# Kernel optimization log

Measured on AMD Instinct MI355X. Metric: run time of the kernel, lower is better.

The kernel has to match this reference:

```python
import jax, jax.numpy as jnp
import numpy as np

B, T, C_IN, H, W = 128, 12, 10, 25, 25
HID = 64
DN = ('NCHW', 'OIHW', 'NCHW')


def setup_inputs() -> dict:
    key = jax.random.key(0)
    ks = jax.random.split(key, 8)
    x = jax.random.normal(ks[0], (B, T, C_IN, H, W), dtype=jnp.float32)
    # ConvLSTM cell: conv over concat([x, h]) -> 4*HID gate channels, 3x3 kernel
    conv_w = jax.random.normal(ks[1], (4 * HID, C_IN + HID, 3, 3), dtype=jnp.float32) * 0.05
    conv_b = jnp.zeros((4 * HID,), dtype=jnp.float32)
    # MLP head: hidden*25*25 -> 16 -> 8 -> 2
    w1 = jax.random.normal(ks[2], (HID * H * W, 16), dtype=jnp.float32) * 0.01
    b1 = jnp.zeros((16,), dtype=jnp.float32)
    w2 = jax.random.normal(ks[3], (16, 8), dtype=jnp.float32) * 0.1
    b2 = jnp.zeros((8,), dtype=jnp.float32)
    w3 = jax.random.normal(ks[4], (8, 2), dtype=jnp.float32) * 0.1
    b3 = jnp.zeros((2,), dtype=jnp.float32)
    return {"x": x, "conv_w": conv_w, "conv_b": conv_b,
            "w1": w1, "b1": b1, "w2": w2, "b2": b2, "w3": w3, "b3": b3}


def _convlstm_last_h(x, conv_w, conv_b):
    # x: (B,T,C,H,W); returns last hidden state h_T: (B,HID,H,W)
    h0 = jnp.zeros((x.shape[0], HID, H, W), dtype=x.dtype)
    c0 = jnp.zeros_like(h0)

    def step(carry, xt):
        h, c = carry
        inp = jnp.concatenate([xt, h], axis=1)              # (B, C+HID, H, W)
        gates = jax.lax.conv_general_dilated(
            inp, conv_w, window_strides=(1, 1), padding='SAME',
            dimension_numbers=DN) + conv_b[None, :, None, None]  # (B,4*HID,H,W)
        i, f, o, g = jnp.split(gates, 4, axis=1)
        i, f, o = jax.nn.sigmoid(i), jax.nn.sigmoid(f), jax.nn.sigmoid(o)
        g = jnp.tanh(g)
        c_new = f * c + i * g
        h_new = o * jnp.tanh(c_new)
        return (h_new, c_new), None

    (h_last, _), _ = jax.lax.scan(step, (h0, c0), jnp.swapaxes(x, 0, 1))
    return h_last


def reference(x, conv_w, conv_b, w1, b1, w2, b2, w3, b3):
    h = _convlstm_last_h(x, conv_w, conv_b)          # (B,HID,25,25)
    h = jax.nn.relu(h).reshape(h.shape[0], -1)       # flatten
    # dropout is identity in eval mode
    h = jax.nn.relu(h @ w1 + b1)
    h = jax.nn.relu(h @ w2 + b2)
    logits = h @ w3 + b3                             # (B,2)
    return jax.nn.log_softmax(logits, axis=1)
```

## Files before the change

kernel.cpp:

```cpp
#include <hip/hip_runtime.h>
#include <hip/hip_bf16.h>
#include <math.h>

#define BATCH 128
#define TT    12
#define CIN   10
#define HID   64
#define PLANE 625
#define NU    10
#define IPB   50000
#define NKB   45
#define CSZ   (BATCH*PLANE*HID)
#define KSPLIT 10

typedef __attribute__((ext_vector_type(8)))  short bf16x8;
typedef __attribute__((ext_vector_type(16))) float f32x16;

__device__ __forceinline__ float fsigm(float v){ return 1.f/(1.f+__expf(-v)); }
__device__ __forceinline__ float ftanh(float v){ return 1.f - 2.f/(__expf(2.f*v)+1.f); }
__device__ __forceinline__ unsigned short f2bf(float v){
    __hip_bfloat16 b = __float2bfloat16(v);
    return *reinterpret_cast<unsigned short*>(&b);
}

__global__ void k_wprep(const float* __restrict__ w, unsigned short* __restrict__ wpk){
    int tid = blockIdx.x*256 + threadIdx.x;
    if (tid >= NKB*8*64) return;
    int lane = tid & 63;
    int nt   = (tid >> 6) & 7;
    int kb   = tid >> 9;
    int tap = kb/5, ci = kb - tap*5;
    int ky = tap/3, kx = tap - ky*3;
    int g = lane & 3, jlo = (lane & 31) >> 2, kh = lane >> 5;
    int o = g*64 + nt*8 + jlo;
    union { unsigned short u[8]; float4 f; } pk;
    #pragma unroll
    for (int e = 0; e < 8; ++e){
        int ch = ci*16 + kh*8 + e;
        float v = (ch < 74) ? w[((o*74 + ch)*3 + ky)*3 + kx] : 0.f;
        pk.u[e] = f2bf(v);
    }
    *reinterpret_cast<float4*>(wpk + (size_t)tid*8) = pk.f;
}

__global__ void k_xcopy(const float* __restrict__ x, unsigned short* __restrict__ inp, int t){
    int idx = blockIdx.x*256 + threadIdx.x;
    if (idx >= BATCH*CIN*PLANE) return;
    int m  = idx % PLANE;
    int r  = idx / PLANE;
    int ch = r % CIN;
    int b  = r / CIN;
    float v = x[((size_t)(b*TT + t)*CIN + ch)*PLANE + m];
    inp[(size_t)b*IPB + ((((ch>>3)*PLANE) + m)<<3) + (ch&7)] = f2bf(v);
}

__global__ __launch_bounds__(512) void k_gemm(
    const float* __restrict__ x,
    const unsigned short* __restrict__ inp,
    unsigned short* __restrict__ inpn,
    const unsigned short* __restrict__ wpk,
    const float* __restrict__ bias,
    float* __restrict__ cbuf,
    float* __restrict__ hbuf,
    int t)
{
    __shared__ __align__(16) unsigned short at2[2160*8];

    const int tid  = threadIdx.x;
    const int mg   = blockIdx.x;
    const int b    = blockIdx.y;
    const int lane = tid & 63;
    const int nt   = tid >> 6;
    const int r0row = (mg*128)/25;

    const unsigned short* ib = inp + (size_t)b*IPB;
    for (int idx = tid; idx < 2160; idx += 512){
        int q   = idx/216, pix = idx - q*216;
        int rr  = pix/27,  cc  = pix - rr*27;
        int gr  = r0row - 1 + rr, gc = cc - 1;
        float4 v = {0.f,0.f,0.f,0.f};
        if ((unsigned)gr < 25u && (unsigned)gc < 25u)
            v = *reinterpret_cast<const float4*>(ib + (((size_t)q*PLANE + gr*25 + gc)<<3));
        *reinterpret_cast<float4*>(at2 + ((size_t)idx<<3)) = v;
    }

    const int kh = lane >> 5;
    const unsigned short* ap[4];
    #pragma unroll
    for (int mt = 0; mt < 4; ++mt){
        int m = mg*128 + mt*32 + (lane & 31);
        int row = m/25, col = m - row*25;
        int pm = (row - r0row + 1)*27 + col;
        ap[mt] = at2 + ((kh*216 + pm - 27) << 3);
    }

    f32x16 acc[4];
    #pragma unroll
    for (int mt = 0; mt < 4; ++mt)
        #pragma unroll
        for (int e = 0; e < 16; ++e) acc[mt][e] = 0.f;

    __syncthreads();

    const bf16x8* wptr = reinterpret_cast<const bf16x8*>(wpk) + nt*64 + lane;
    bf16x8 bcur = *wptr;
    const unsigned short *a0 = ap[0], *a1 = ap[1], *a2 = ap[2], *a3 = ap[3];
    #pragma unroll 1
    for (int tap = 0; tap < 9; ++tap){
        #pragma unroll
        for (int ci = 0; ci < 5; ++ci){
            bf16x8 bnxt = wptr[512];
            wptr += 512;
            bf16x8 f0 = *reinterpret_cast<const bf16x8*>(a0 + ci*3456);
            bf16x8 f1 = *reinterpret_cast<const bf16x8*>(a1 + ci*3456);
            bf16x8 f2 = *reinterpret_cast<const bf16x8*>(a2 + ci*3456);
            bf16x8 f3 = *reinterpret_cast<const bf16x8*>(a3 + ci*3456);
            acc[0] = __builtin_amdgcn_mfma_f32_32x32x16_bf16(f0, bcur, acc[0], 0,0,0);
            acc[1] = __builtin_amdgcn_mfma_f32_32x32x16_bf16(f1, bcur, acc[1], 0,0,0);
            acc[2] = __builtin_amdgcn_mfma_f32_32x32x16_bf16(f2, bcur, acc[2], 0,0,0);
            acc[3] = __builtin_amdgcn_mfma_f32_32x32x16_bf16(f3, bcur, acc[3], 0,0,0);
            bcur = bnxt;
        }
        const int d = (tap == 2 || tap == 5) ? 25*8 : 8;
        a0 += d; a1 += d; a2 += d; a3 += d;
    }

    const int g   = lane & 3;
    const int jlo = (lane & 31) >> 2;
    const int j   = nt*8 + jlo;
    const float bown = bias[g*64 + j];
    const float sA = (g == 3) ? 2.f : 1.f;
    const float sB = (g == 3) ? -1.f : 0.f;
    const int  mbase = mg*128 + 4*kh;
    const bool gb0 = (g & 1), gb1 = (g & 2);
    float* cb = cbuf + (size_t)b*PLANE*HID;
    float* hb = hbuf + (size_t)b*PLANE*HID;
    unsigned short* hn = inpn + (size_t)b*IPB;
    const int chh = CIN + j, uh = chh >> 3, sh = chh & 7;

    #pragma unroll
    for (int mt = 0; mt < 4; ++mt){
        #pragma unroll
        for (int rq = 0; rq < 4; ++rq){
            float v0 = fmaf(sA, fsigm(sA*(acc[mt][rq*4+0] + bown)), sB);
            float v1 = fmaf(sA, fsigm(sA*(acc[mt][rq*4+1] + bown)), sB);
            float v2 = fmaf(sA, fsigm(sA*(acc[mt][rq*4+2] + bown)), sB);
            float v3 = fmaf(sA, fsigm(sA*(acc[mt][rq*4+3] + bown)), sB);
            float s;
            s = __shfl_xor(gb0 ? v0 : v1, 1); if (gb0) v0 = s; else v1 = s;
            s = __shfl_xor(gb0 ? v2 : v3, 1); if (gb0) v2 = s; else v3 = s;
            s = __shfl_xor(gb1 ? v0 : v2, 2); if (gb1) v0 = s; else v2 = s;
            s = __shfl_xor(gb1 ? v1 : v3, 2); if (gb1) v1 = s; else v3 = s;
            const int m = mbase + mt*32 + g + 8*rq;
            if (m < PLANE){
                float co = cb[m*HID + j];
                float cn = fmaf(v1, co, v0*v3);
                float h  = v2 * ftanh(cn);
                cb[m*HID + j] = cn;
                hn[((uh*PLANE + m) << 3) + sh] = f2bf(h);
                if (t == TT-1) hb[m*HID + j] = h;
            }
        }
    }

    if (t < TT-1){
        const float* xn = x + (size_t)(b*TT + t + 1)*CIN*PLANE;
        for (int idx = tid; idx < 1280; idx += 512){
            int ch = idx >> 7, mi = idx & 127;
            int m = mg*128 + mi;
            if (m < PLANE)
                inpn[(size_t)b*IPB + ((((ch>>3)*PLANE) + m)<<3) + (ch&7)] =
                    f2bf(xn[ch*PLANE + m]);
        }
    }
}

__global__ __launch_bounds__(256) void k_mlp1(
    const float* __restrict__ hfin, const float* __restrict__ w1,
    float* __restrict__ part)
{
    __shared__ float xw[4][16];
    const int ks = blockIdx.x, b = blockIdx.y, tid = threadIdx.x;
    const float* hbb = hfin + (size_t)b * (HID * PLANE);

    float acc[16];
    #pragma unroll
    for (int i = 0; i < 16; ++i) acc[i] = 0.f;

    const int kw0 = ks * 4000, kw1 = kw0 + 4000;
    for (int kw = kw0 + tid; kw < kw1; kw += 256){
        int j = kw / 625, m = kw - j * 625;
        float hv = hbb[m * 64 + j];
        hv = hv > 0.f ? hv : 0.f;
        const float4* wf = (const float4*)(w1 + (size_t)kw * 16);
        float4 wa = wf[0], wb = wf[1], wc = wf[2], wd = wf[3];
        acc[ 0] = fmaf(hv, wa.x, acc[ 0]); acc[ 1] = fmaf(hv, wa.y, acc[ 1]);
        acc[ 2] = fmaf(hv, wa.z, acc[ 2]); acc[ 3] = fmaf(hv, wa.w, acc[ 3]);
        acc[ 4] = fmaf(hv, wb.x, acc[ 4]); acc[ 5] = fmaf(hv, wb.y, acc[ 5]);
        acc[ 6] = fmaf(hv, wb.z, acc[ 6]); acc[ 7] = fmaf(hv, wb.w, acc[ 7]);
        acc[ 8] = fmaf(hv, wc.x, acc[ 8]); acc[ 9] = fmaf(hv, wc.y, acc[ 9]);
        acc[10] = fmaf(hv, wc.z, acc[10]); acc[11] = fmaf(hv, wc.w, acc[11]);
        acc[12] = fmaf(hv, wd.x, acc[12]); acc[13] = fmaf(hv, wd.y, acc[13]);
        acc[14] = fmaf(hv, wd.z, acc[14]); acc[15] = fmaf(hv, wd.w, acc[15]);
    }
    #pragma unroll
    for (int d = 1; d < 64; d <<= 1)
        #pragma unroll
        for (int i = 0; i < 16; ++i) acc[i] += __shfl_xor(acc[i], d);
    if ((tid & 63) == 0)
        #pragma unroll
        for (int i = 0; i < 16; ++i) xw[tid >> 6][i] = acc[i];
    __syncthreads();
    if (tid < 16)
        part[((size_t)b * KSPLIT + ks) * 16 + tid] =
            xw[0][tid] + xw[1][tid] + xw[2][tid] + xw[3][tid];
}

__global__ __launch_bounds__(128) void k_mlp2(
    const float* __restrict__ part,
    const float* __restrict__ b1,
    const float* __restrict__ w2, const float* __restrict__ b2,
    const float* __restrict__ w3, const float* __restrict__ b3,
    float* __restrict__ out)
{
    const int b = threadIdx.x;
    float h1[16];
    #pragma unroll
    for (int i = 0; i < 16; ++i) h1[i] = b1[i];
    for (int s = 0; s < KSPLIT; ++s)
        #pragma unroll
        for (int i = 0; i < 16; ++i) h1[i] += part[((size_t)b * KSPLIT + s) * 16 + i];
    #pragma unroll
    for (int i = 0; i < 16; ++i) h1[i] = h1[i] > 0.f ? h1[i] : 0.f;

    float h2[8];
    #pragma unroll
    for (int i = 0; i < 8; ++i){
        float s2 = b2[i];
        #pragma unroll
        for (int k2 = 0; k2 < 16; ++k2) s2 += h1[k2] * w2[k2*8 + i];
        h2[i] = s2 > 0.f ? s2 : 0.f;
    }
    float l0 = b3[0], l1 = b3[1];
    #pragma unroll
    for (int k3 = 0; k3 < 8; ++k3){ l0 += h2[k3]*w3[k3*2]; l1 += h2[k3]*w3[k3*2+1]; }
    float m   = fmaxf(l0, l1);
    float lse = m + logf(__expf(l0 - m) + __expf(l1 - m));
    out[b*2 + 0] = l0 - lse;
    out[b*2 + 1] = l1 - lse;
}

extern "C" void kernel_launch(void* const* d_in, const int* in_sizes, int n_in,
                              void* d_out, int out_size, void* d_ws, size_t ws_size,
                              hipStream_t stream) {
    const float* x      = (const float*)d_in[0];
    const float* conv_w = (const float*)d_in[1];
    const float* conv_b = (const float*)d_in[2];
    const float* w1     = (const float*)d_in[3];
    const float* b1     = (const float*)d_in[4];
    const float* w2     = (const float*)d_in[5];
    const float* b2     = (const float*)d_in[6];
    const float* w3     = (const float*)d_in[7];
    const float* b3     = (const float*)d_in[8];
    float* out = (float*)d_out;

    unsigned short* inp0 = (unsigned short*)d_ws;
    unsigned short* inp1 = inp0 + (size_t)BATCH*IPB;
    float* c   = (float*)(inp1 + (size_t)BATCH*IPB);
    float* hb  = c + CSZ;
    unsigned short* wpk = (unsigned short*)(hb + CSZ);
    float* part = (float*)(wpk + (size_t)(NKB+1)*8*64*8);

    hipMemsetAsync(inp0, 0, (size_t)BATCH*IPB*2, stream);
    hipMemsetAsync(inp1, 0, (size_t)BATCH*IPB*2, stream);
    hipMemsetAsync(c,    0, (size_t)CSZ*4,       stream);

    k_wprep<<<dim3(90),   dim3(256), 0, stream>>>(conv_w, wpk);
    k_xcopy<<<dim3(3125), dim3(256), 0, stream>>>(x, inp0, 0);

    for (int t = 0; t < TT; ++t){
        unsigned short* ic  = (t & 1) ? inp1 : inp0;
        unsigned short* in_ = (t & 1) ? inp0 : inp1;
        k_gemm<<<dim3(5, BATCH), dim3(512), 0, stream>>>(x, ic, in_, wpk, conv_b, c, hb, t);
    }
    k_mlp1<<<dim3(KSPLIT, BATCH), dim3(256), 0, stream>>>(hb, w1, part);
    k_mlp2<<<dim3(1), dim3(128), 0, stream>>>(part, b1, w2, b2, w3, b3, out);
}
```

Before: 732.9 us.

## Halve gemm pixel tile, store bf16 relu'd final h, batch MLP1 over four samples

The ConvLSTM gemm now covers 64 pixels per block instead of 128, doubling the grid to 10x128 blocks and shrinking the LDS tile. This raises occupancy and parallelism for the recurrent step. The last timestep writes only a bf16, ReLU-applied hidden state in pixel-major order and skips the useless c/h updates. w1 is pre-permuted to match that layout, so k_mlp1 reads it contiguously and reuses each weight load across four batch samples. The costs are more halo reloads per block and an extra prep kernel, plus bf16 rounding of the MLP input.

```diff
diff --git a/kernel.cpp b/kernel.cpp
--- a/kernel.cpp
+++ b/kernel.cpp
@@ -43,6 +43,15 @@
     *reinterpret_cast<float4*>(wpk + (size_t)tid*8) = pk.f;
 }
 
+__global__ void k_w1prep(const float* __restrict__ w1, float* __restrict__ w1t){
+    int tid = blockIdx.x*256 + threadIdx.x;
+    if (tid >= 40000*4) return;
+    int rowp = tid >> 2, f4 = tid & 3;
+    int m = rowp >> 6, j = rowp & 63;
+    const float4* src = (const float4*)(w1 + (size_t)(j*625 + m)*16);
+    ((float4*)(w1t + (size_t)rowp*16))[f4] = src[f4];
+}
+
 __global__ void k_xcopy(const float* __restrict__ x, unsigned short* __restrict__ inp, int t){
     int idx = blockIdx.x*256 + threadIdx.x;
     if (idx >= BATCH*CIN*PLANE) return;
@@ -61,23 +70,23 @@
     const unsigned short* __restrict__ wpk,
     const float* __restrict__ bias,
     float* __restrict__ cbuf,
-    float* __restrict__ hbuf,
+    unsigned short* __restrict__ hbf,
     int t)
 {
-    __shared__ __align__(16) unsigned short at2[2160*8];
+    __shared__ __align__(16) unsigned short at2[1620*8];
 
     const int tid  = threadIdx.x;
     const int mg   = blockIdx.x;
     const int b    = blockIdx.y;
     const int lane = tid & 63;
     const int nt   = tid >> 6;
-    const int r0row = (mg*128)/25;
+    const int rlo  = (mg*64)/25;
 
     const unsigned short* ib = inp + (size_t)b*IPB;
-    for (int idx = tid; idx < 2160; idx += 512){
-        int q   = idx/216, pix = idx - q*216;
+    for (int idx = tid; idx < 1620; idx += 512){
+        int q   = idx/162, pix = idx - q*162;
         int rr  = pix/27,  cc  = pix - rr*27;
-        int gr  = r0row - 1 + rr, gc = cc - 1;
+        int gr  = rlo - 1 + rr, gc = cc - 1;
         float4 v = {0.f,0.f,0.f,0.f};
         if ((unsigned)gr < 25u && (unsigned)gc < 25u)
             v = *reinterpret_cast<const float4*>(ib + (((size_t)q*PLANE + gr*25 + gc)<<3));
@@ -85,18 +94,18 @@
     }
 
     const int kh = lane >> 5;
-    const unsigned short* ap[4];
-    #pragma unroll
-    for (int mt = 0; mt < 4; ++mt){
-        int m = mg*128 + mt*32 + (lane & 31);
+    const unsigned short* ap[2];
+    #pragma unroll
+    for (int mt = 0; mt < 2; ++mt){
+        int m = mg*64 + mt*32 + (lane & 31);
         int row = m/25, col = m - row*25;
-        int pm = (row - r0row + 1)*27 + col;
-        ap[mt] = at2 + ((kh*216 + pm - 27) << 3);
-    }
-
-    f32x16 acc[4];
-    #pragma unroll
-    for (int mt = 0; mt < 4; ++mt)
+        int pm = (row - rlo + 1)*27 + col;
+        ap[mt] = at2 + kh*1296 + ((pm - 27) << 3);
+    }
+
+    f32x16 acc[2];
+    #pragma unroll
+    for (int mt = 0; mt < 2; ++mt)
         #pragma unroll
         for (int e = 0; e < 16; ++e) acc[mt][e] = 0.f;
 
@@ -104,25 +113,21 @@
 
     const bf16x8* wptr = reinterpret_cast<const bf16x8*>(wpk) + nt*64 + lane;
     bf16x8 bcur = *wptr;
-    const unsigned short *a0 = ap[0], *a1 = ap[1], *a2 = ap[2], *a3 = ap[3];
+    const unsigned short *a0 = ap[0], *a1 = ap[1];
     #pragma unroll 1
     for (int tap = 0; tap < 9; ++tap){
         #pragma unroll
         for (int ci = 0; ci < 5; ++ci){
             bf16x8 bnxt = wptr[512];
             wptr += 512;
-            bf16x8 f0 = *reinterpret_cast<const bf16x8*>(a0 + ci*3456);
-            bf16x8 f1 = *reinterpret_cast<const bf16x8*>(a1 + ci*3456);
-            bf16x8 f2 = *reinterpret_cast<const bf16x8*>(a2 + ci*3456);
-            bf16x8 f3 = *reinterpret_cast<const bf16x8*>(a3 + ci*3456);
+            bf16x8 f0 = *reinterpret_cast<const bf16x8*>(a0 + ci*2592);
+            bf16x8 f1 = *reinterpret_cast<const bf16x8*>(a1 + ci*2592);
             acc[0] = __builtin_amdgcn_mfma_f32_32x32x16_bf16(f0, bcur, acc[0], 0,0,0);
             acc[1] = __builtin_amdgcn_mfma_f32_32x32x16_bf16(f1, bcur, acc[1], 0,0,0);
-            acc[2] = __builtin_amdgcn_mfma_f32_32x32x16_bf16(f2, bcur, acc[2], 0,0,0);
-            acc[3] = __builtin_amdgcn_mfma_f32_32x32x16_bf16(f3, bcur, acc[3], 0,0,0);
             bcur = bnxt;
         }
         const int d = (tap == 2 || tap == 5) ? 25*8 : 8;
-        a0 += d; a1 += d; a2 += d; a3 += d;
+        a0 += d; a1 += d;
     }
 
     const int g   = lane & 3;
@@ -131,15 +136,15 @@
     const float bown = bias[g*64 + j];
     const float sA = (g == 3) ? 2.f : 1.f;
     const float sB = (g == 3) ? -1.f : 0.f;
-    const int  mbase = mg*128 + 4*kh;
+    const int  mbase = mg*64 + 4*kh;
     const bool gb0 = (g & 1), gb1 = (g & 2);
     float* cb = cbuf + (size_t)b*PLANE*HID;
-    float* hb = hbuf + (size_t)b*PLANE*HID;
-    unsigned short* hn = inpn + (size_t)b*IPB;
+    unsigned short* hn  = inpn + (size_t)b*IPB;
+    unsigned short* hfb = hbf  + (size_t)b*40000;
     const int chh = CIN + j, uh = chh >> 3, sh = chh & 7;
 
     #pragma unroll
-    for (int mt = 0; mt < 4; ++mt){
+    for (int mt = 0; mt < 2; ++mt){
         #pragma unroll
         for (int rq = 0; rq < 4; ++rq){
             float v0 = fmaf(sA, fsigm(sA*(acc[mt][rq*4+0] + bown)), sB);
@@ -156,18 +161,21 @@
                 float co = cb[m*HID + j];
                 float cn = fmaf(v1, co, v0*v3);
                 float h  = v2 * ftanh(cn);
-                cb[m*HID + j] = cn;
-                hn[((uh*PLANE + m) << 3) + sh] = f2bf(h);
-                if (t == TT-1) hb[m*HID + j] = h;
+                if (t < TT-1){
+                    cb[m*HID + j] = cn;
+                    hn[((uh*PLANE + m) << 3) + sh] = f2bf(h);
+                } else {
+                    hfb[m*64 + j] = f2bf(h > 0.f ? h : 0.f);
+                }
             }
         }
     }
 
     if (t < TT-1){
         const float* xn = x + (size_t)(b*TT + t + 1)*CIN*PLANE;
-        for (int idx = tid; idx < 1280; idx += 512){
-            int ch = idx >> 7, mi = idx & 127;
-            int m = mg*128 + mi;
+        for (int idx = tid; idx < 640; idx += 512){
+            int ch = idx >> 6, mi = idx & 63;
+            int m = mg*64 + mi;
             if (m < PLANE)
                 inpn[(size_t)b*IPB + ((((ch>>3)*PLANE) + m)<<3) + (ch&7)] =
                     f2bf(xn[ch*PLANE + m]);
@@ -176,44 +184,73 @@
 }
 
 __global__ __launch_bounds__(256) void k_mlp1(
-    const float* __restrict__ hfin, const float* __restrict__ w1,
+    const unsigned short* __restrict__ hbf, const float* __restrict__ w1t,
     float* __restrict__ part)
 {
-    __shared__ float xw[4][16];
-    const int ks = blockIdx.x, b = blockIdx.y, tid = threadIdx.x;
-    const float* hbb = hfin + (size_t)b * (HID * PLANE);
-
-    float acc[16];
-    #pragma unroll
-    for (int i = 0; i < 16; ++i) acc[i] = 0.f;
-
-    const int kw0 = ks * 4000, kw1 = kw0 + 4000;
-    for (int kw = kw0 + tid; kw < kw1; kw += 256){
-        int j = kw / 625, m = kw - j * 625;
-        float hv = hbb[m * 64 + j];
-        hv = hv > 0.f ? hv : 0.f;
-        const float4* wf = (const float4*)(w1 + (size_t)kw * 16);
-        float4 wa = wf[0], wb = wf[1], wc = wf[2], wd = wf[3];
-        acc[ 0] = fmaf(hv, wa.x, acc[ 0]); acc[ 1] = fmaf(hv, wa.y, acc[ 1]);
-        acc[ 2] = fmaf(hv, wa.z, acc[ 2]); acc[ 3] = fmaf(hv, wa.w, acc[ 3]);
-        acc[ 4] = fmaf(hv, wb.x, acc[ 4]); acc[ 5] = fmaf(hv, wb.y, acc[ 5]);
-        acc[ 6] = fmaf(hv, wb.z, acc[ 6]); acc[ 7] = fmaf(hv, wb.w, acc[ 7]);
-        acc[ 8] = fmaf(hv, wc.x, acc[ 8]); acc[ 9] = fmaf(hv, wc.y, acc[ 9]);
-        acc[10] = fmaf(hv, wc.z, acc[10]); acc[11] = fmaf(hv, wc.w, acc[11]);
-        acc[12] = fmaf(hv, wd.x, acc[12]); acc[13] = fmaf(hv, wd.y, acc[13]);
-        acc[14] = fmaf(hv, wd.z, acc[14]); acc[15] = fmaf(hv, wd.w, acc[15]);
-    }
+    __shared__ float xw[4][4][16];
+    const int ks = blockIdx.x, bg = blockIdx.y, tid = threadIdx.x;
+    const int kw0 = ks*4000, kw1 = kw0 + 4000;
+    const unsigned short* h0 = hbf + (size_t)(bg*4+0)*40000;
+    const unsigned short* h1 = hbf + (size_t)(bg*4+1)*40000;
+    const unsigned short* h2 = hbf + (size_t)(bg*4+2)*40000;
+    const unsigned short* h3 = hbf + (size_t)(bg*4+3)*40000;
+
+    float acc[4][16];
+    #pragma unroll
+    for (int bi = 0; bi < 4; ++bi)
+        #pragma unroll
+        for (int n = 0; n < 16; ++n) acc[bi][n] = 0.f;
+
+    for (int kw = kw0 + tid*2; kw < kw1; kw += 512){
+        const float4* wp = (const float4*)(w1t + (size_t)kw*16);
+        float4 q0 = wp[0], q1 = wp[1], q2 = wp[2], q3 = wp[3];
+        float4 r0 = wp[4], r1 = wp[5], r2 = wp[6], r3 = wp[7];
+        unsigned int u0 = *(const unsigned int*)(h0 + kw);
+        unsigned int u1 = *(const unsigned int*)(h1 + kw);
+        unsigned int u2 = *(const unsigned int*)(h2 + kw);
+        unsigned int u3 = *(const unsigned int*)(h3 + kw);
+        #define ACC1(bi, u) { \
+            float fl = __uint_as_float((u) << 16); \
+            float fh = __uint_as_float((u) & 0xffff0000u); \
+            acc[bi][ 0]=fmaf(fl,q0.x,fmaf(fh,r0.x,acc[bi][ 0])); \
+            acc[bi][ 1]=fmaf(fl,q0.y,fmaf(fh,r0.y,acc[bi][ 1])); \
+            acc[bi][ 2]=fmaf(fl,q0.z,fmaf(fh,r0.z,acc[bi][ 2])); \
+            acc[bi][ 3]=fmaf(fl,q0.w,fmaf(fh,r0.w,acc[bi][ 3])); \
+            acc[bi][ 4]=fmaf(fl,q1.x,fmaf(fh,r1.x,acc[bi][ 4])); \
+            acc[bi][ 5]=fmaf(fl,q1.y,fmaf(fh,r1.y,acc[bi][ 5])); \
+            acc[bi][ 6]=fmaf(fl,q1.z,fmaf(fh,r1.z,acc[bi][ 6])); \
+            acc[bi][ 7]=fmaf(fl,q1.w,fmaf(fh,r1.w,acc[bi][ 7])); \
+            acc[bi][ 8]=fmaf(fl,q2.x,fmaf(fh,r2.x,acc[bi][ 8])); \
+            acc[bi][ 9]=fmaf(fl,q2.y,fmaf(fh,r2.y,acc[bi][ 9])); \
+            acc[bi][10]=fmaf(fl,q2.z,fmaf(fh,r2.z,acc[bi][10])); \
+            acc[bi][11]=fmaf(fl,q2.w,fmaf(fh,r2.w,acc[bi][11])); \
+            acc[bi][12]=fmaf(fl,q3.x,fmaf(fh,r3.x,acc[bi][12])); \
+            acc[bi][13]=fmaf(fl,q3.y,fmaf(fh,r3.y,acc[bi][13])); \
+            acc[bi][14]=fmaf(fl,q3.z,fmaf(fh,r3.z,acc[bi][14])); \
+            acc[bi][15]=fmaf(fl,q3.w,fmaf(fh,r3.w,acc[bi][15])); }
+        ACC1(0, u0) ACC1(1, u1) ACC1(2, u2) ACC1(3, u3)
+        #undef ACC1
+    }
+
     #pragma unroll
     for (int d = 1; d < 64; d <<= 1)
         #pragma unroll
-        for (int i = 0; i < 16; ++i) acc[i] += __shfl_xor(acc[i], d);
-    if ((tid & 63) == 0)
-        #pragma unroll
-        for (int i = 0; i < 16; ++i) xw[tid >> 6][i] = acc[i];
+        for (int bi = 0; bi < 4; ++bi)
+            #pragma unroll
+            for (int n = 0; n < 16; ++n) acc[bi][n] += __shfl_xor(acc[bi][n], d);
+    if ((tid & 63) == 0){
+        int w = tid >> 6;
+        #pragma unroll
+        for (int bi = 0; bi < 4; ++bi)
+            #pragma unroll
+            for (int n = 0; n < 16; ++n) xw[w][bi][n] = acc[bi][n];
+    }
     __syncthreads();
-    if (tid < 16)
-        part[((size_t)b * KSPLIT + ks) * 16 + tid] =
-            xw[0][tid] + xw[1][tid] + xw[2][tid] + xw[3][tid];
+    if (tid < 64){
+        int bi = tid >> 4, n = tid & 15;
+        float s = xw[0][bi][n] + xw[1][bi][n] + xw[2][bi][n] + xw[3][bi][n];
+        part[((size_t)(bg*4 + bi)*KSPLIT + ks)*16 + n] = s;
+    }
 }
 
 __global__ __launch_bounds__(128) void k_mlp2(
@@ -267,22 +304,24 @@
     unsigned short* inp0 = (unsigned short*)d_ws;
     unsigned short* inp1 = inp0 + (size_t)BATCH*IPB;
     float* c   = (float*)(inp1 + (size_t)BATCH*IPB);
-    float* hb  = c + CSZ;
-    unsigned short* wpk = (unsigned short*)(hb + CSZ);
-    float* part = (float*)(wpk + (size_t)(NKB+1)*8*64*8);
+    unsigned short* hbf = (unsigned short*)(c + CSZ);
+    unsigned short* wpk = hbf + (size_t)BATCH*40000;
+    float* w1t  = (float*)(wpk + (size_t)(NKB+1)*8*64*8);
+    float* part = w1t + 640000;
 
     hipMemsetAsync(inp0, 0, (size_t)BATCH*IPB*2, stream);
     hipMemsetAsync(inp1, 0, (size_t)BATCH*IPB*2, stream);
     hipMemsetAsync(c,    0, (size_t)CSZ*4,       stream);
 
-    k_wprep<<<dim3(90),   dim3(256), 0, stream>>>(conv_w, wpk);
-    k_xcopy<<<dim3(3125), dim3(256), 0, stream>>>(x, inp0, 0);
+    k_wprep <<<dim3(90),   dim3(256), 0, stream>>>(conv_w, wpk);
+    k_w1prep<<<dim3(625),  dim3(256), 0, stream>>>(w1, w1t);
+    k_xcopy <<<dim3(3125), dim3(256), 0, stream>>>(x, inp0, 0);
 
     for (int t = 0; t < TT; ++t){
         unsigned short* ic  = (t & 1) ? inp1 : inp0;
         unsigned short* in_ = (t & 1) ? inp0 : inp1;
-        k_gemm<<<dim3(5, BATCH), dim3(512), 0, stream>>>(x, ic, in_, wpk, conv_b, c, hb, t);
-    }
-    k_mlp1<<<dim3(KSPLIT, BATCH), dim3(256), 0, stream>>>(hb, w1, part);
+        k_gemm<<<dim3(10, BATCH), dim3(512), 0, stream>>>(x, ic, in_, wpk, conv_b, c, hbf, t);
+    }
+    k_mlp1<<<dim3(KSPLIT, 32), dim3(256), 0, stream>>>(hbf, w1t, part);
     k_mlp2<<<dim3(1), dim3(128), 0, stream>>>(part, b1, w2, b2, w3, b3, out);
 }
```

Result: faster. 625.0 us, median of 4 (-14.7%).
